# Performance work log

Measured on AMD Instinct MI355X. Metric: run time of the kernel, lower is better.

## Reference

```python
import jax, jax.numpy as jnp
import numpy as np
from jax import lax

B = 8192      # image batch
S = 32        # seq_length
I = 16        # ltc_input_size (sensory neurons)
U = 19        # ltc_hidden_size (units)
M = 2         # num_classes (motor neurons)
UNFOLDS = 6   # ncps LTCCell default ode_unfolds
EPS = 1e-8


def setup_inputs() -> dict:
    key = jax.random.key(0)
    ks = jax.random.split(key, 24)
    u = lambda k, sh, lo, hi: jax.random.uniform(k, sh, jnp.float32, lo, hi)
    x = jax.random.normal(ks[0], (B, 1, 28, 44), jnp.float32)
    conv1_w = jax.random.normal(ks[1], (6, 1, 5, 5), jnp.float32) * 0.2
    conv1_b = u(ks[2], (6,), -0.1, 0.1)
    conv2_w = jax.random.normal(ks[3], (16, 6, 5, 5), jnp.float32) * 0.08
    conv2_b = u(ks[4], (16,), -0.1, 0.1)
    # wiring adjacency (AutoNCP approximated by random sparse +/-1 polarity)
    sparsity_mask = (jax.random.uniform(ks[5], (U, U)) < 0.5).astype(jnp.float32)
    sensory_sparsity_mask = (jax.random.uniform(ks[6], (I, U)) < 0.5).astype(jnp.float32)
    erev = sparsity_mask * jnp.where(jax.random.uniform(ks[7], (U, U)) < 0.8, 1.0, -1.0)
    sensory_erev = sensory_sparsity_mask * jnp.where(jax.random.uniform(ks[8], (I, U)) < 0.8, 1.0, -1.0)
    # LTCCell parameter init ranges from ncps
    gleak = u(ks[9], (U,), 0.001, 1.0)
    vleak = u(ks[10], (U,), -0.2, 0.2)
    cm = u(ks[11], (U,), 0.4, 0.6)
    sigma = u(ks[12], (U, U), 3.0, 8.0)
    mu = u(ks[13], (U, U), 0.3, 0.8)
    w = u(ks[14], (U, U), 0.001, 1.0)
    sensory_sigma = u(ks[15], (I, U), 3.0, 8.0)
    sensory_mu = u(ks[16], (I, U), 0.3, 0.8)
    sensory_w = u(ks[17], (I, U), 0.001, 1.0)
    input_w = jnp.ones((I,), jnp.float32)
    input_b = jnp.zeros((I,), jnp.float32)
    output_w = jnp.ones((M,), jnp.float32)
    output_b = jnp.zeros((M,), jnp.float32)
    return dict(x=x, conv1_w=conv1_w, conv1_b=conv1_b, conv2_w=conv2_w, conv2_b=conv2_b,
                gleak=gleak, vleak=vleak, cm=cm, sigma=sigma, mu=mu, w=w, erev=erev,
                sensory_sigma=sensory_sigma, sensory_mu=sensory_mu, sensory_w=sensory_w,
                sensory_erev=sensory_erev, input_w=input_w, input_b=input_b,
                output_w=output_w, output_b=output_b,
                sparsity_mask=sparsity_mask, sensory_sparsity_mask=sensory_sparsity_mask)


def _maxpool2(h):
    return lax.reduce_window(h, -jnp.inf, lax.max, (1, 1, 2, 2), (1, 1, 2, 2), 'VALID')


def reference(x, conv1_w, conv1_b, conv2_w, conv2_b, gleak, vleak, cm, sigma, mu, w,
              erev, sensory_sigma, sensory_mu, sensory_w, sensory_erev, input_w, input_b,
              output_w, output_b, sparsity_mask, sensory_sparsity_mask):
    dn = ('NCHW', 'OIHW', 'NCHW')
    h = lax.conv_general_dilated(x, conv1_w, (1, 1), 'VALID', dimension_numbers=dn)
    h = _maxpool2(jax.nn.relu(h + conv1_b[None, :, None, None]))
    h = lax.conv_general_dilated(h, conv2_w, (1, 1), 'VALID', dimension_numbers=dn)
    h = _maxpool2(jax.nn.relu(h + conv2_b[None, :, None, None]))
    feat = h.reshape(h.shape[0], -1).reshape(-1, S, I)   # (B, 32, 16)
    seq = jnp.swapaxes(feat, 0, 1)                       # (S, B, I)
    cm_t = cm * UNFOLDS                                  # cm / (elapsed_time/unfolds), dt=1

    def step(v, inp):
        inp = inp * input_w + input_b                    # sensory affine mapping
        # sensory synapse activations (B, I, U), fixed over the ODE unfolds
        s_act = sensory_w * jax.nn.sigmoid(sensory_sigma * (inp[:, :, None] - sensory_mu))
        s_act = s_act * sensory_sparsity_mask
        w_num_s = jnp.sum(s_act * sensory_erev, axis=1)
        w_den_s = jnp.sum(s_act, axis=1)

        def unfold(vv, _):
            wa = w * jax.nn.sigmoid(sigma * (vv[:, :, None] - mu)) * sparsity_mask  # (B,U,U)
            num = cm_t * vv + gleak * vleak + jnp.sum(wa * erev, axis=1) + w_num_s
            den = cm_t + gleak + jnp.sum(wa, axis=1) + w_den_s
            return num / (den + EPS), None

        v, _ = lax.scan(unfold, v, None, length=UNFOLDS)
        return v, None

    v0 = jnp.zeros((feat.shape[0], U), x.dtype)
    vT, _ = lax.scan(step, v0, seq)
    # motor mapping: first M neurons, affine output map; equals out[:, -1, :]
    return vT[:, :M] * output_w + output_b
```

## Files before the change

### kernel.cpp

```cpp
#include <hip/hip_runtime.h>

#define BTOT 8192
#define SEQ 32
#define IPB 6
#define TPB 128
#define L2E 1.4426950408889634f
#define FSTRIDE 520
#define VSTRIDE 20

__global__ void prep_w2t(const float* __restrict__ w2, float* __restrict__ wt) {
    int idx = blockIdx.x * blockDim.x + threadIdx.x;
    if (idx < 2400) {
        int k = idx >> 4, c2 = idx & 15;
        wt[idx] = w2[c2 * 150 + k];
    }
}

__global__ __launch_bounds__(TPB, 3) void ltc_fused(
    const float* __restrict__ xin,
    const float* __restrict__ w1, const float* __restrict__ b1,
    const float* __restrict__ b2,
    const float* __restrict__ gleak, const float* __restrict__ vleak, const float* __restrict__ cm,
    const float* __restrict__ sigma, const float* __restrict__ mu, const float* __restrict__ ww,
    const float* __restrict__ erev,
    const float* __restrict__ ssigma, const float* __restrict__ smu, const float* __restrict__ sw,
    const float* __restrict__ serev,
    const float* __restrict__ inw, const float* __restrict__ inb,
    const float* __restrict__ outw, const float* __restrict__ outb,
    const float* __restrict__ wt,
    float* __restrict__ dout)
{
    __shared__ __align__(16) float uni[2672];
    __shared__ __align__(16) float featL[IPB * FSTRIDE];
    __shared__ __align__(16) float vbuf[IPB * VSTRIDE];

    float* img = uni;
    float* c1p = uni + 1232;
    float* uA = uni;
    float* uB = uni + 361;
    float* uZ = uni + 722;
    float* sA = uni + 1083;
    float* sB = uni + 1387;
    float* sZ = uni + 1691;

    const int tid = threadIdx.x;
    const int b0 = blockIdx.x * IPB;

    for (int k = 0; k < IPB; ++k) {
        const int bG = b0 + k;
        const bool valid = bG < BTOT;
        if (valid) {
            for (int idx = tid; idx < 1232; idx += TPB) img[idx] = xin[bG * 1232 + idx];
        }
        __syncthreads();
        if (valid) {
            for (int idx = tid; idx < 240; idx += TPB) {
                int y = idx / 20, xx = idx - (idx / 20) * 20;
                const float* ib = img + (2 * y) * 44 + 2 * xx;
                float win[6][6];
                #pragma unroll
                for (int r = 0; r < 6; ++r) {
                    float2 a = *(const float2*)(ib + r * 44);
                    float2 b = *(const float2*)(ib + r * 44 + 2);
                    float2 c = *(const float2*)(ib + r * 44 + 4);
                    win[r][0] = a.x; win[r][1] = a.y; win[r][2] = b.x;
                    win[r][3] = b.y; win[r][4] = c.x; win[r][5] = c.y;
                }
                for (int ch = 0; ch < 6; ++ch) {
                    const float* wp = w1 + ch * 25;
                    float a00 = 0.f, a01 = 0.f, a10 = 0.f, a11 = 0.f;
                    #pragma unroll
                    for (int ky = 0; ky < 5; ++ky)
                        #pragma unroll
                        for (int kx = 0; kx < 5; ++kx) {
                            float wv = wp[ky * 5 + kx];
                            a00 = fmaf(wv, win[ky][kx], a00);
                            a01 = fmaf(wv, win[ky][kx + 1], a01);
                            a10 = fmaf(wv, win[ky + 1][kx], a10);
                            a11 = fmaf(wv, win[ky + 1][kx + 1], a11);
                        }
                    float m = fmaxf(fmaxf(a00, a01), fmaxf(a10, a11)) + b1[ch];
                    c1p[ch * 240 + idx] = fmaxf(m, 0.f);
                }
            }
        }
        __syncthreads();
        if (valid) {
            const int oy = tid >> 4, ox = tid & 15;
            float acc[16];
            #pragma unroll
            for (int c2 = 0; c2 < 16; ++c2) acc[c2] = 0.f;
            for (int ch = 0; ch < 6; ++ch) {
                const float* rowb = c1p + ch * 240 + oy * 20 + ox;
                const float* wch = wt + (ch * 25 << 4);
                #pragma unroll
                for (int ky = 0; ky < 5; ++ky) {
                    #pragma unroll
                    for (int kx = 0; kx < 5; ++kx) {
                        float xv = rowb[ky * 20 + kx];
                        const float4* wk = (const float4*)(wch + ((ky * 5 + kx) << 4));
                        float4 wa = wk[0], wb = wk[1], wc = wk[2], wd = wk[3];
                        acc[0]  = fmaf(wa.x, xv, acc[0]);  acc[1]  = fmaf(wa.y, xv, acc[1]);
                        acc[2]  = fmaf(wa.z, xv, acc[2]);  acc[3]  = fmaf(wa.w, xv, acc[3]);
                        acc[4]  = fmaf(wb.x, xv, acc[4]);  acc[5]  = fmaf(wb.y, xv, acc[5]);
                        acc[6]  = fmaf(wb.z, xv, acc[6]);  acc[7]  = fmaf(wb.w, xv, acc[7]);
                        acc[8]  = fmaf(wc.x, xv, acc[8]);  acc[9]  = fmaf(wc.y, xv, acc[9]);
                        acc[10] = fmaf(wc.z, xv, acc[10]); acc[11] = fmaf(wc.w, xv, acc[11]);
                        acc[12] = fmaf(wd.x, xv, acc[12]); acc[13] = fmaf(wd.y, xv, acc[13]);
                        acc[14] = fmaf(wd.z, xv, acc[14]); acc[15] = fmaf(wd.w, xv, acc[15]);
                    }
                }
            }
            const bool wl = ((tid & 1) == 0) && ((tid & 16) == 0);
            const int obase = k * FSTRIDE + (oy >> 1) * 8 + (ox >> 1);
            #pragma unroll
            for (int c2 = 0; c2 < 16; ++c2) {
                float a = acc[c2];
                a = fmaxf(a, __shfl_xor(a, 1));
                a = fmaxf(a, __shfl_xor(a, 16));
                if (wl) featL[obase + c2 * 32] = fmaxf(a + b2[c2], 0.f);
            }
        }
        __syncthreads();
    }

    for (int idx = tid; idx < 665; idx += TPB) {
        if (idx < 361) {
            float s = sigma[idx];
            uA[idx] = -L2E * s;
            uB[idx] = L2E * s * mu[idx];
            uZ[idx] = ww[idx] * erev[idx];
        } else {
            int kk = idx - 361;
            int i = kk / 19;
            float s = ssigma[kk];
            sA[kk] = -L2E * s * inw[i];
            sB[kk] = -L2E * s * (inb[i] - smu[kk]);
            sZ[kk] = sw[kk] * serev[kk];
        }
    }
    for (int idx = tid; idx < IPB * VSTRIDE; idx += TPB) vbuf[idx] = 0.f;
    __syncthreads();

    const int wv_ = tid >> 6, l = tid & 63;
    const int g = l / 19;
    const int j = l - g * 19;
    const int kimg = wv_ * 3 + g;
    const bool act = (g < 3) && (b0 + kimg < BTOT);
    const int kc = (kimg < IPB) ? kimg : (IPB - 1);

    float UA[19], UB[19], UZ[19];
    #pragma unroll
    for (int i = 0; i < 19; ++i) {
        UA[i] = uA[i * 19 + j];
        UB[i] = uB[i * 19 + j];
        UZ[i] = uZ[i * 19 + j];
    }
    #pragma unroll
    for (int i = 0; i < 19; ++i)
        asm volatile("" : "+v"(UA[i]), "+v"(UB[i]), "+v"(UZ[i]));

    float gl = gleak[j];
    float gv = gl * vleak[j];
    float cmt = cm[j] * 6.f;
    asm volatile("" : "+v"(gl), "+v"(gv), "+v"(cmt));

    float v = 0.f;
    const float* sAj = sA + j;
    const float* sBj = sB + j;
    const float* sZj = sZ + j;

    for (int s = 0; s < SEQ; ++s) {
        const float4* fb4 = (const float4*)(featL + kc * FSTRIDE + s * 16);
        float4 f0 = fb4[0], f1 = fb4[1], f2 = fb4[2], f3 = fb4[3];
        float fv[16] = {f0.x,f0.y,f0.z,f0.w, f1.x,f1.y,f1.z,f1.w,
                        f2.x,f2.y,f2.z,f2.w, f3.x,f3.y,f3.z,f3.w};
        float wns = 0.f, wds = 0.f;
        #pragma unroll
        for (int i = 0; i < 16; ++i) {
            float t = fmaf(sAj[i * 19], fv[i], sBj[i * 19]);
            float r = __builtin_amdgcn_rcpf(1.f + __builtin_amdgcn_exp2f(t));
            float z = sZj[i * 19];
            wns = fmaf(z, r, wns);
            wds = fmaf(fabsf(z), r, wds);
        }
        const float nb = gv + wns;
        const float db = cmt + gl + wds;
        #pragma unroll 1
        for (int u = 0; u < 6; ++u) {
            const float4* vb4 = (const float4*)(vbuf + kc * VSTRIDE);
            float4 va = vb4[0], vb = vb4[1], vc = vb4[2], vd = vb4[3], ve = vb4[4];
            float vv[19] = {va.x,va.y,va.z,va.w, vb.x,vb.y,vb.z,vb.w,
                            vc.x,vc.y,vc.z,vc.w, vd.x,vd.y,vd.z,vd.w,
                            ve.x,ve.y,ve.z};
            float num = fmaf(cmt, v, nb);
            float den = db;
            #pragma unroll
            for (int i = 0; i < 19; ++i) {
                float t = fmaf(UA[i], vv[i], UB[i]);
                float r = __builtin_amdgcn_rcpf(1.f + __builtin_amdgcn_exp2f(t));
                num = fmaf(UZ[i], r, num);
                den = fmaf(fabsf(UZ[i]), r, den);
            }
            v = num * __builtin_amdgcn_rcpf(den + 1e-8f);
            __builtin_amdgcn_wave_barrier();
            __asm__ volatile("" ::: "memory");
            if (act) vbuf[kimg * VSTRIDE + j] = v;
            __builtin_amdgcn_wave_barrier();
            __asm__ volatile("" ::: "memory");
        }
    }
    if (act && j < 2) dout[(b0 + kimg) * 2 + j] = fmaf(v, outw[j], outb[j]);
}

extern "C" void kernel_launch(void* const* d_in, const int* in_sizes, int n_in,
                              void* d_out, int out_size, void* d_ws, size_t ws_size,
                              hipStream_t stream) {
    const float* x      = (const float*)d_in[0];
    const float* w1     = (const float*)d_in[1];
    const float* b1     = (const float*)d_in[2];
    const float* w2     = (const float*)d_in[3];
    const float* b2     = (const float*)d_in[4];
    const float* gleak  = (const float*)d_in[5];
    const float* vleak  = (const float*)d_in[6];
    const float* cm     = (const float*)d_in[7];
    const float* sigma  = (const float*)d_in[8];
    const float* mu     = (const float*)d_in[9];
    const float* ww     = (const float*)d_in[10];
    const float* erev   = (const float*)d_in[11];
    const float* ssig   = (const float*)d_in[12];
    const float* smu    = (const float*)d_in[13];
    const float* sw     = (const float*)d_in[14];
    const float* serev  = (const float*)d_in[15];
    const float* inw    = (const float*)d_in[16];
    const float* inb    = (const float*)d_in[17];
    const float* outw   = (const float*)d_in[18];
    const float* outb   = (const float*)d_in[19];
    float* wt = (float*)d_ws;

    hipLaunchKernelGGL(prep_w2t, dim3(10), dim3(256), 0, stream, w2, wt);

    dim3 grid((BTOT + IPB - 1) / IPB), block(TPB);
    hipLaunchKernelGGL(ltc_fused, grid, block, 0, stream,
                       x, w1, b1, b2, gleak, vleak, cm, sigma, mu, ww, erev,
                       ssig, smu, sw, serev, inw, inb, outw, outb,
                       (const float*)wt, (float*)d_out);
}
```

Baseline: 318.8 us.

## Split LTC synapse sums across lane groups with one image per wavefront

The LTC recurrence changes from three images per wavefront, with one lane per neuron summing all 19 presynaptic inputs, to one image per wavefront. Three 19-lane groups each handle a slice of about 7 recurrent and 6 sensory presynaptic inputs, and the partial sums are combined with cross-lane shuffles. Block size goes to 256 threads with 4 images per block, and conv2 output channels are split between the two halves of the block. The aim is to shorten the serial dependency chain per ODE unfold and raise occupancy, at the cost of extra shuffles and more lanes spent per image.

```diff
diff --git a/kernel.cpp b/kernel.cpp
--- a/kernel.cpp
+++ b/kernel.cpp
@@ -2,8 +2,8 @@
 
 #define BTOT 8192
 #define SEQ 32
-#define IPB 6
-#define TPB 128
+#define IPB 4
+#define TPB 256
 #define L2E 1.4426950408889634f
 #define FSTRIDE 520
 #define VSTRIDE 20
@@ -16,7 +16,7 @@
     }
 }
 
-__global__ __launch_bounds__(TPB, 3) void ltc_fused(
+__global__ __launch_bounds__(TPB, 5) void ltc_fused(
     const float* __restrict__ xin,
     const float* __restrict__ w1, const float* __restrict__ b1,
     const float* __restrict__ b2,
@@ -48,76 +48,70 @@
 
     for (int k = 0; k < IPB; ++k) {
         const int bG = b0 + k;
-        const bool valid = bG < BTOT;
-        if (valid) {
-            for (int idx = tid; idx < 1232; idx += TPB) img[idx] = xin[bG * 1232 + idx];
-        }
+        for (int idx = tid; idx < 1232; idx += TPB) img[idx] = xin[bG * 1232 + idx];
         __syncthreads();
-        if (valid) {
-            for (int idx = tid; idx < 240; idx += TPB) {
-                int y = idx / 20, xx = idx - (idx / 20) * 20;
-                const float* ib = img + (2 * y) * 44 + 2 * xx;
-                float win[6][6];
+        if (tid < 240) {
+            const int y = tid / 20, xx = tid - (tid / 20) * 20;
+            const float* ib = img + (2 * y) * 44 + 2 * xx;
+            float win[6][6];
+            #pragma unroll
+            for (int r = 0; r < 6; ++r) {
+                float2 a = *(const float2*)(ib + r * 44);
+                float2 b = *(const float2*)(ib + r * 44 + 2);
+                float2 c = *(const float2*)(ib + r * 44 + 4);
+                win[r][0] = a.x; win[r][1] = a.y; win[r][2] = b.x;
+                win[r][3] = b.y; win[r][4] = c.x; win[r][5] = c.y;
+            }
+            for (int ch = 0; ch < 6; ++ch) {
+                const float* wp = w1 + ch * 25;
+                float a00 = 0.f, a01 = 0.f, a10 = 0.f, a11 = 0.f;
                 #pragma unroll
-                for (int r = 0; r < 6; ++r) {
-                    float2 a = *(const float2*)(ib + r * 44);
-                    float2 b = *(const float2*)(ib + r * 44 + 2);
-                    float2 c = *(const float2*)(ib + r * 44 + 4);
-                    win[r][0] = a.x; win[r][1] = a.y; win[r][2] = b.x;
-                    win[r][3] = b.y; win[r][4] = c.x; win[r][5] = c.y;
-                }
-                for (int ch = 0; ch < 6; ++ch) {
-                    const float* wp = w1 + ch * 25;
-                    float a00 = 0.f, a01 = 0.f, a10 = 0.f, a11 = 0.f;
+                for (int ky = 0; ky < 5; ++ky)
                     #pragma unroll
-                    for (int ky = 0; ky < 5; ++ky)
-                        #pragma unroll
-                        for (int kx = 0; kx < 5; ++kx) {
-                            float wv = wp[ky * 5 + kx];
-                            a00 = fmaf(wv, win[ky][kx], a00);
-                            a01 = fmaf(wv, win[ky][kx + 1], a01);
-                            a10 = fmaf(wv, win[ky + 1][kx], a10);
-                            a11 = fmaf(wv, win[ky + 1][kx + 1], a11);
-                        }
-                    float m = fmaxf(fmaxf(a00, a01), fmaxf(a10, a11)) + b1[ch];
-                    c1p[ch * 240 + idx] = fmaxf(m, 0.f);
-                }
+                    for (int kx = 0; kx < 5; ++kx) {
+                        float wv = wp[ky * 5 + kx];
+                        a00 = fmaf(wv, win[ky][kx], a00);
+                        a01 = fmaf(wv, win[ky][kx + 1], a01);
+                        a10 = fmaf(wv, win[ky + 1][kx], a10);
+                        a11 = fmaf(wv, win[ky + 1][kx + 1], a11);
+                    }
+                float m = fmaxf(fmaxf(a00, a01), fmaxf(a10, a11)) + b1[ch];
+                c1p[ch * 240 + tid] = fmaxf(m, 0.f);
             }
         }
         __syncthreads();
-        if (valid) {
-            const int oy = tid >> 4, ox = tid & 15;
-            float acc[16];
-            #pragma unroll
-            for (int c2 = 0; c2 < 16; ++c2) acc[c2] = 0.f;
+        {
+            const int half = tid >> 7;
+            const int pos = tid & 127;
+            const int oy = pos >> 4, ox = pos & 15;
+            float acc[8];
+            #pragma unroll
+            for (int c = 0; c < 8; ++c) acc[c] = 0.f;
             for (int ch = 0; ch < 6; ++ch) {
                 const float* rowb = c1p + ch * 240 + oy * 20 + ox;
-                const float* wch = wt + (ch * 25 << 4);
+                const float* wch = wt + (ch * 25 << 4) + (half << 3);
                 #pragma unroll
                 for (int ky = 0; ky < 5; ++ky) {
                     #pragma unroll
                     for (int kx = 0; kx < 5; ++kx) {
                         float xv = rowb[ky * 20 + kx];
                         const float4* wk = (const float4*)(wch + ((ky * 5 + kx) << 4));
-                        float4 wa = wk[0], wb = wk[1], wc = wk[2], wd = wk[3];
-                        acc[0]  = fmaf(wa.x, xv, acc[0]);  acc[1]  = fmaf(wa.y, xv, acc[1]);
-                        acc[2]  = fmaf(wa.z, xv, acc[2]);  acc[3]  = fmaf(wa.w, xv, acc[3]);
-                        acc[4]  = fmaf(wb.x, xv, acc[4]);  acc[5]  = fmaf(wb.y, xv, acc[5]);
-                        acc[6]  = fmaf(wb.z, xv, acc[6]);  acc[7]  = fmaf(wb.w, xv, acc[7]);
-                        acc[8]  = fmaf(wc.x, xv, acc[8]);  acc[9]  = fmaf(wc.y, xv, acc[9]);
-                        acc[10] = fmaf(wc.z, xv, acc[10]); acc[11] = fmaf(wc.w, xv, acc[11]);
-                        acc[12] = fmaf(wd.x, xv, acc[12]); acc[13] = fmaf(wd.y, xv, acc[13]);
-                        acc[14] = fmaf(wd.z, xv, acc[14]); acc[15] = fmaf(wd.w, xv, acc[15]);
+                        float4 wa = wk[0], wb = wk[1];
+                        acc[0] = fmaf(wa.x, xv, acc[0]); acc[1] = fmaf(wa.y, xv, acc[1]);
+                        acc[2] = fmaf(wa.z, xv, acc[2]); acc[3] = fmaf(wa.w, xv, acc[3]);
+                        acc[4] = fmaf(wb.x, xv, acc[4]); acc[5] = fmaf(wb.y, xv, acc[5]);
+                        acc[6] = fmaf(wb.z, xv, acc[6]); acc[7] = fmaf(wb.w, xv, acc[7]);
                     }
                 }
             }
             const bool wl = ((tid & 1) == 0) && ((tid & 16) == 0);
             const int obase = k * FSTRIDE + (oy >> 1) * 8 + (ox >> 1);
             #pragma unroll
-            for (int c2 = 0; c2 < 16; ++c2) {
-                float a = acc[c2];
+            for (int c = 0; c < 8; ++c) {
+                float a = acc[c];
                 a = fmaxf(a, __shfl_xor(a, 1));
                 a = fmaxf(a, __shfl_xor(a, 16));
+                int c2 = (half << 3) + c;
                 if (wl) featL[obase + c2 * 32] = fmaxf(a + b2[c2], 0.f);
             }
         }
@@ -139,78 +133,88 @@
             sZ[kk] = sw[kk] * serev[kk];
         }
     }
-    for (int idx = tid; idx < IPB * VSTRIDE; idx += TPB) vbuf[idx] = 0.f;
+    if (tid < IPB * VSTRIDE) vbuf[tid] = 0.f;
     __syncthreads();
 
-    const int wv_ = tid >> 6, l = tid & 63;
-    const int g = l / 19;
-    const int j = l - g * 19;
-    const int kimg = wv_ * 3 + g;
-    const bool act = (g < 3) && (b0 + kimg < BTOT);
-    const int kc = (kimg < IPB) ? kimg : (IPB - 1);
-
-    float UA[19], UB[19], UZ[19];
-    #pragma unroll
-    for (int i = 0; i < 19; ++i) {
-        UA[i] = uA[i * 19 + j];
-        UB[i] = uB[i * 19 + j];
-        UZ[i] = uZ[i * 19 + j];
-    }
-    #pragma unroll
-    for (int i = 0; i < 19; ++i)
-        asm volatile("" : "+v"(UA[i]), "+v"(UB[i]), "+v"(UZ[i]));
-
-    float gl = gleak[j];
-    float gv = gl * vleak[j];
-    float cmt = cm[j] * 6.f;
-    asm volatile("" : "+v"(gl), "+v"(gv), "+v"(cmt));
+    const int wv = tid >> 6, l = tid & 63;
+    const int sb3 = l / 19;
+    const int sb = (sb3 < 2) ? sb3 : 2;
+    const int j = l - sb3 * 19;
+    const int imgi = b0 + wv;
+    const int ibr = (sb == 0) ? 0 : ((sb == 1) ? 7 : 13);
+    const int ibs = (sb == 0) ? 0 : ((sb == 1) ? 6 : 11);
+
+    float UA[7], UB[7], UZ[7], SA[6], SB[6], SZ[6];
+    #pragma unroll
+    for (int c = 0; c < 7; ++c) {
+        int ig = ibr + c;
+        bool pad = (sb > 0 && c == 6);
+        int idx = ((ig < 19) ? ig : 18) * 19 + j;
+        UA[c] = pad ? 0.f : uA[idx];
+        UB[c] = pad ? 0.f : uB[idx];
+        UZ[c] = pad ? 0.f : uZ[idx];
+    }
+    #pragma unroll
+    for (int c = 0; c < 6; ++c) {
+        int ig = ibs + c;
+        bool pad = (sb > 0 && c == 5);
+        int idx = ((ig < 16) ? ig : 15) * 19 + j;
+        SA[c] = pad ? 0.f : sA[idx];
+        SB[c] = pad ? 0.f : sB[idx];
+        SZ[c] = pad ? 0.f : sZ[idx];
+    }
+    #pragma unroll
+    for (int c = 0; c < 7; ++c) asm volatile("" : "+v"(UA[c]), "+v"(UB[c]), "+v"(UZ[c]));
+    #pragma unroll
+    for (int c = 0; c < 6; ++c) asm volatile("" : "+v"(SA[c]), "+v"(SB[c]), "+v"(SZ[c]));
+
+    const float gl = gleak[j];
+    const float gv = gl * vleak[j];
+    const float cmt = cm[j] * 6.f;
 
     float v = 0.f;
-    const float* sAj = sA + j;
-    const float* sBj = sB + j;
-    const float* sZj = sZ + j;
-
-    for (int s = 0; s < SEQ; ++s) {
-        const float4* fb4 = (const float4*)(featL + kc * FSTRIDE + s * 16);
-        float4 f0 = fb4[0], f1 = fb4[1], f2 = fb4[2], f3 = fb4[3];
-        float fv[16] = {f0.x,f0.y,f0.z,f0.w, f1.x,f1.y,f1.z,f1.w,
-                        f2.x,f2.y,f2.z,f2.w, f3.x,f3.y,f3.z,f3.w};
-        float wns = 0.f, wds = 0.f;
+    const float* frow = featL + wv * FSTRIDE;
+    const float* vrow = vbuf + wv * VSTRIDE;
+
+    for (int st = 0; st < SEQ; ++st) {
+        const float* fb = frow + st * 16 + ibs;
+        float wnp = 0.f, wdp = 0.f;
         #pragma unroll
-        for (int i = 0; i < 16; ++i) {
-            float t = fmaf(sAj[i * 19], fv[i], sBj[i * 19]);
+        for (int c = 0; c < 6; ++c) {
+            float t = fmaf(SA[c], fb[c], SB[c]);
             float r = __builtin_amdgcn_rcpf(1.f + __builtin_amdgcn_exp2f(t));
-            float z = sZj[i * 19];
-            wns = fmaf(z, r, wns);
-            wds = fmaf(fabsf(z), r, wds);
-        }
+            wnp = fmaf(SZ[c], r, wnp);
+            wdp = fmaf(fabsf(SZ[c]), r, wdp);
+        }
+        float wns = wnp + __shfl(wnp, l + 19) + __shfl(wnp, l + 38);
+        float wds = wdp + __shfl(wdp, l + 19) + __shfl(wdp, l + 38);
         const float nb = gv + wns;
         const float db = cmt + gl + wds;
+
         #pragma unroll 1
         for (int u = 0; u < 6; ++u) {
-            const float4* vb4 = (const float4*)(vbuf + kc * VSTRIDE);
-            float4 va = vb4[0], vb = vb4[1], vc = vb4[2], vd = vb4[3], ve = vb4[4];
-            float vv[19] = {va.x,va.y,va.z,va.w, vb.x,vb.y,vb.z,vb.w,
-                            vc.x,vc.y,vc.z,vc.w, vd.x,vd.y,vd.z,vd.w,
-                            ve.x,ve.y,ve.z};
-            float num = fmaf(cmt, v, nb);
-            float den = db;
-            #pragma unroll
-            for (int i = 0; i < 19; ++i) {
-                float t = fmaf(UA[i], vv[i], UB[i]);
+            float pn = 0.f, pd = 0.f;
+            const float* vr = vrow + ibr;
+            #pragma unroll
+            for (int c = 0; c < 7; ++c) {
+                float t = fmaf(UA[c], vr[c], UB[c]);
                 float r = __builtin_amdgcn_rcpf(1.f + __builtin_amdgcn_exp2f(t));
-                num = fmaf(UZ[i], r, num);
-                den = fmaf(fabsf(UZ[i]), r, den);
-            }
+                pn = fmaf(UZ[c], r, pn);
+                pd = fmaf(fabsf(UZ[c]), r, pd);
+            }
+            pn += __shfl(pn, l + 19) + __shfl(pn, l + 38);
+            pd += __shfl(pd, l + 19) + __shfl(pd, l + 38);
+            float num = fmaf(cmt, v, nb) + pn;
+            float den = db + pd;
             v = num * __builtin_amdgcn_rcpf(den + 1e-8f);
             __builtin_amdgcn_wave_barrier();
             __asm__ volatile("" ::: "memory");
-            if (act) vbuf[kimg * VSTRIDE + j] = v;
+            if (l < 19) vbuf[wv * VSTRIDE + j] = v;
             __builtin_amdgcn_wave_barrier();
             __asm__ volatile("" ::: "memory");
         }
     }
-    if (act && j < 2) dout[(b0 + kimg) * 2 + j] = fmaf(v, outw[j], outb[j]);
+    if (l < 2) dout[imgi * 2 + l] = fmaf(v, outw[l], outb[l]);
 }
 
 extern "C" void kernel_launch(void* const* d_in, const int* in_sizes, int n_in,
@@ -240,7 +244,7 @@
 
     hipLaunchKernelGGL(prep_w2t, dim3(10), dim3(256), 0, stream, w2, wt);
 
-    dim3 grid((BTOT + IPB - 1) / IPB), block(TPB);
+    dim3 grid(BTOT / IPB), block(TPB);
     hipLaunchKernelGGL(ltc_fused, grid, block, 0, stream,
                        x, w1, b1, b2, gleak, vleak, cm, sigma, mu, ww, erev,
                        ssig, smu, sw, serev, inw, inb, outw, outb,
```

New measurement: 398.7 us. 1.25x slower.

## Compact synapse lists by sparsity mask and pair sigmoids to share reciprocals

Applied to the files above, without the earlier changes.

Builds per-neuron compacted lists of nonzero synapses, from the sparsity masks, in shared memory as float4 records holding the coefficients and a byte offset. The ODE and sensory loops then iterate only over active synapses, padded to an even count. Sigmoids are processed in pairs so one reciprocal serves two terms. In exchange, the fully unrolled register-resident weights become runtime-bounded LDS-indexed loops with gather loads, and paired reciprocals may lose precision or overflow when exp2 is large.

```diff
diff --git a/kernel.cpp b/kernel.cpp
--- a/kernel.cpp
+++ b/kernel.cpp
@@ -27,21 +27,19 @@
     const float* __restrict__ serev,
     const float* __restrict__ inw, const float* __restrict__ inb,
     const float* __restrict__ outw, const float* __restrict__ outb,
+    const float* __restrict__ mask, const float* __restrict__ smask,
     const float* __restrict__ wt,
     float* __restrict__ dout)
 {
-    __shared__ __align__(16) float uni[2672];
+    __shared__ __align__(16) float uni[2736];
     __shared__ __align__(16) float featL[IPB * FSTRIDE];
     __shared__ __align__(16) float vbuf[IPB * VSTRIDE];
+    __shared__ int ncol[19], mcol[19], cnts[2];
 
     float* img = uni;
     float* c1p = uni + 1232;
-    float* uA = uni;
-    float* uB = uni + 361;
-    float* uZ = uni + 722;
-    float* sA = uni + 1083;
-    float* sB = uni + 1387;
-    float* sZ = uni + 1691;
+    float4* cR = (float4*)uni;
+    float4* cS = ((float4*)uni) + 20 * 19;
 
     const int tid = threadIdx.x;
     const int b0 = blockIdx.x * IPB;
@@ -124,23 +122,48 @@
         __syncthreads();
     }
 
-    for (int idx = tid; idx < 665; idx += TPB) {
-        if (idx < 361) {
-            float s = sigma[idx];
-            uA[idx] = -L2E * s;
-            uB[idx] = L2E * s * mu[idx];
-            uZ[idx] = ww[idx] * erev[idx];
-        } else {
-            int kk = idx - 361;
-            int i = kk / 19;
-            float s = ssigma[kk];
-            sA[kk] = -L2E * s * inw[i];
-            sB[kk] = -L2E * s * (inb[i] - smu[kk]);
-            sZ[kk] = sw[kk] * serev[kk];
-        }
-    }
-    for (int idx = tid; idx < IPB * VSTRIDE; idx += TPB) vbuf[idx] = 0.f;
+    for (int idx = tid; idx < 2736; idx += TPB) uni[idx] = 0.f;
+    if (tid < IPB * VSTRIDE) vbuf[tid] = 0.f;
     __syncthreads();
+    if (tid < 19) {
+        const int j = tid;
+        int c = 0;
+        for (int i = 0; i < 19; ++i) {
+            int idx = i * 19 + j;
+            if (mask[idx] != 0.f) {
+                float s = sigma[idx];
+                cR[c * 19 + j] = make_float4(-L2E * s, L2E * s * mu[idx],
+                                             ww[idx] * erev[idx], __int_as_float(i * 4));
+                ++c;
+            }
+        }
+        ncol[j] = c;
+        c = 0;
+        for (int i = 0; i < 16; ++i) {
+            int idx = i * 19 + j;
+            if (smask[idx] != 0.f) {
+                float s = ssigma[idx];
+                cS[c * 19 + j] = make_float4(-L2E * s * inw[i],
+                                             -L2E * s * (inb[i] - smu[idx]),
+                                             sw[idx] * serev[idx], __int_as_float(i * 4));
+                ++c;
+            }
+        }
+        mcol[j] = c;
+    }
+    __syncthreads();
+    if (tid == 0) {
+        int MR = 0, MS = 0;
+        for (int j2 = 0; j2 < 19; ++j2) {
+            MR = max(MR, ncol[j2]);
+            MS = max(MS, mcol[j2]);
+        }
+        cnts[0] = (MR + 1) & ~1;
+        cnts[1] = (MS + 1) & ~1;
+    }
+    __syncthreads();
+    const int MR = __builtin_amdgcn_readfirstlane(cnts[0]);
+    const int MS = __builtin_amdgcn_readfirstlane(cnts[1]);
 
     const int wv_ = tid >> 6, l = tid & 63;
     const int g = l / 19;
@@ -149,58 +172,55 @@
     const bool act = (g < 3) && (b0 + kimg < BTOT);
     const int kc = (kimg < IPB) ? kimg : (IPB - 1);
 
-    float UA[19], UB[19], UZ[19];
-    #pragma unroll
-    for (int i = 0; i < 19; ++i) {
-        UA[i] = uA[i * 19 + j];
-        UB[i] = uB[i * 19 + j];
-        UZ[i] = uZ[i * 19 + j];
-    }
-    #pragma unroll
-    for (int i = 0; i < 19; ++i)
-        asm volatile("" : "+v"(UA[i]), "+v"(UB[i]), "+v"(UZ[i]));
-
-    float gl = gleak[j];
-    float gv = gl * vleak[j];
-    float cmt = cm[j] * 6.f;
-    asm volatile("" : "+v"(gl), "+v"(gv), "+v"(cmt));
+    const float gl = gleak[j];
+    const float gv = gl * vleak[j];
+    const float cmt = cm[j] * 6.f;
 
     float v = 0.f;
-    const float* sAj = sA + j;
-    const float* sBj = sB + j;
-    const float* sZj = sZ + j;
-
-    for (int s = 0; s < SEQ; ++s) {
-        const float4* fb4 = (const float4*)(featL + kc * FSTRIDE + s * 16);
-        float4 f0 = fb4[0], f1 = fb4[1], f2 = fb4[2], f3 = fb4[3];
-        float fv[16] = {f0.x,f0.y,f0.z,f0.w, f1.x,f1.y,f1.z,f1.w,
-                        f2.x,f2.y,f2.z,f2.w, f3.x,f3.y,f3.z,f3.w};
+    const char* frowb = (const char*)(featL + kc * FSTRIDE);
+    const char* vrowb = (const char*)(vbuf + kc * VSTRIDE);
+
+    #pragma unroll 1
+    for (int st = 0; st < SEQ; ++st) {
+        const char* fb = frowb + (st << 6);
         float wns = 0.f, wds = 0.f;
-        #pragma unroll
-        for (int i = 0; i < 16; ++i) {
-            float t = fmaf(sAj[i * 19], fv[i], sBj[i * 19]);
-            float r = __builtin_amdgcn_rcpf(1.f + __builtin_amdgcn_exp2f(t));
-            float z = sZj[i * 19];
-            wns = fmaf(z, r, wns);
-            wds = fmaf(fabsf(z), r, wds);
+        #pragma unroll 1
+        for (int c = 0; c < MS; c += 2) {
+            float4 pa = cS[c * 19 + j];
+            float4 pb = cS[(c + 1) * 19 + j];
+            float fa = *(const float*)(fb + __float_as_int(pa.w));
+            float fbv = *(const float*)(fb + __float_as_int(pb.w));
+            float ta = fmaf(pa.x, fa, pa.y);
+            float tb = fmaf(pb.x, fbv, pb.y);
+            float qa = 1.f + __builtin_amdgcn_exp2f(ta);
+            float qb = 1.f + __builtin_amdgcn_exp2f(tb);
+            float rr = __builtin_amdgcn_rcpf(qa * qb);
+            float cn = fmaf(pa.z, qb, pb.z * qa);
+            float cd = fmaf(fabsf(pa.z), qb, fabsf(pb.z) * qa);
+            wns = fmaf(cn, rr, wns);
+            wds = fmaf(cd, rr, wds);
         }
         const float nb = gv + wns;
         const float db = cmt + gl + wds;
         #pragma unroll 1
         for (int u = 0; u < 6; ++u) {
-            const float4* vb4 = (const float4*)(vbuf + kc * VSTRIDE);
-            float4 va = vb4[0], vb = vb4[1], vc = vb4[2], vd = vb4[3], ve = vb4[4];
-            float vv[19] = {va.x,va.y,va.z,va.w, vb.x,vb.y,vb.z,vb.w,
-                            vc.x,vc.y,vc.z,vc.w, vd.x,vd.y,vd.z,vd.w,
-                            ve.x,ve.y,ve.z};
             float num = fmaf(cmt, v, nb);
             float den = db;
-            #pragma unroll
-            for (int i = 0; i < 19; ++i) {
-                float t = fmaf(UA[i], vv[i], UB[i]);
-                float r = __builtin_amdgcn_rcpf(1.f + __builtin_amdgcn_exp2f(t));
-                num = fmaf(UZ[i], r, num);
-                den = fmaf(fabsf(UZ[i]), r, den);
+            #pragma unroll 1
+            for (int c = 0; c < MR; c += 2) {
+                float4 pa = cR[c * 19 + j];
+                float4 pb = cR[(c + 1) * 19 + j];
+                float va = *(const float*)(vrowb + __float_as_int(pa.w));
+                float vb = *(const float*)(vrowb + __float_as_int(pb.w));
+                float ta = fmaf(pa.x, va, pa.y);
+                float tb = fmaf(pb.x, vb, pb.y);
+                float qa = 1.f + __builtin_amdgcn_exp2f(ta);
+                float qb = 1.f + __builtin_amdgcn_exp2f(tb);
+                float rr = __builtin_amdgcn_rcpf(qa * qb);
+                float cn = fmaf(pa.z, qb, pb.z * qa);
+                float cd = fmaf(fabsf(pa.z), qb, fabsf(pb.z) * qa);
+                num = fmaf(cn, rr, num);
+                den = fmaf(cd, rr, den);
             }
             v = num * __builtin_amdgcn_rcpf(den + 1e-8f);
             __builtin_amdgcn_wave_barrier();
@@ -236,6 +256,8 @@
     const float* inb    = (const float*)d_in[17];
     const float* outw   = (const float*)d_in[18];
     const float* outb   = (const float*)d_in[19];
+    const float* mask   = (const float*)d_in[20];
+    const float* smask  = (const float*)d_in[21];
     float* wt = (float*)d_ws;
 
     hipLaunchKernelGGL(prep_w2t, dim3(10), dim3(256), 0, stream, w2, wt);
@@ -243,6 +265,6 @@
     dim3 grid((BTOT + IPB - 1) / IPB), block(TPB);
     hipLaunchKernelGGL(ltc_fused, grid, block, 0, stream,
                        x, w1, b1, b2, gleak, vleak, cm, sigma, mu, ww, erev,
-                       ssig, smu, sw, serev, inw, inb, outw, outb,
+                       ssig, smu, sw, serev, inw, inb, outw, outb, mask, smask,
                        (const float*)wt, (float*)d_out);
 }
```

Result: slower. 359.6 us (+12.8%).
